# Kernel tuning notes

Measured on AMD Instinct MI355X. Metric: run time of the kernel, lower is better.

## Reference

```python
import jax, jax.numpy as jnp
import numpy as np

B, N, E, D = 8, 10000, 160000, 256
H = D // 2
SLOPE = 0.2  # LeakyReLU negative slope


def setup_inputs() -> dict:
    key = jax.random.key(0)
    ks = jax.random.split(key, 8)
    node_feats = jax.random.normal(ks[0], (B, N, D), dtype=jnp.float32)
    edge_attr = jax.random.uniform(ks[1], (E, 1), dtype=jnp.float32)
    W1 = jax.random.normal(ks[2], (2 * D, H), dtype=jnp.float32) * 0.05
    b1 = jnp.zeros((H,), dtype=jnp.float32)
    W2 = jax.random.normal(ks[3], (H, 1), dtype=jnp.float32) * 0.05
    b2 = jnp.zeros((1,), dtype=jnp.float32)
    edge_index = jax.random.randint(ks[4], (2, E), 0, N, dtype=jnp.int64)
    valid_masks = jax.random.randint(ks[5], (B, N), 0, 2).astype(bool)
    return {"node_feats": node_feats, "edge_attr": edge_attr, "W1": W1, "b1": b1,
            "W2": W2, "b2": b2, "edge_index": edge_index, "valid_masks": valid_masks}


def reference(node_feats, edge_attr, W1, b1, W2, b2, edge_index, valid_masks):
    # node_feats: [B,N,D]; edge_index: [2,E] shared across batch
    d = node_feats.shape[-1]
    src, dst = edge_index[0], edge_index[1]
    # cat([src_feats, dst_feats]) @ W1 == src @ W1[:d] + dst @ W1[d:]
    # Project per-node first, then gather per-edge: avoids the [B,E,2D] concat.
    ps = jnp.einsum('bnd,dh->bnh', node_feats, W1[:d])   # [B,N,H]
    pd = jnp.einsum('bnd,dh->bnh', node_feats, W1[d:])   # [B,N,H]
    h = ps[:, src] + pd[:, dst] + b1                      # [B,E,H]
    h = jnp.where(h >= 0, h, SLOPE * h)                   # LeakyReLU(0.2)
    scores = jnp.einsum('beh,h->be', h, W2[:, 0]) + b2[0]  # [B,E]
    scores = scores * edge_attr[:, 0]                     # edge_attr multiplies pre-softmax
    w = jax.nn.softmax(scores, axis=1)                    # global softmax over all edges
    # sparse_coo(edge_index, w) @ node_feats: out[src[e]] += w[e] * feats[dst[e]]
    msg = w[..., None] * node_feats[:, dst]               # [B,E,D]
    n = node_feats.shape[1]
    agg = jax.vmap(lambda m: jax.ops.segment_sum(m, src, num_segments=n))(msg)  # [B,N,D]
    mask = valid_masks.astype(node_feats.dtype)           # [B,N]
    cnt = mask.sum(axis=1)                                # [B]
    masked_mean = (agg * mask[..., None]).sum(axis=1) / jnp.maximum(cnt, 1.0)[:, None]
    full_mean = agg.mean(axis=1)
    graph_feats = jnp.where((cnt > 0)[:, None], masked_mean, full_mean)  # [B,D]
    return graph_feats, w
```

## Files before the change

kernel.cpp:

```cpp
#include <hip/hip_runtime.h>
#include <hip/hip_bf16.h>
#include <hip/hip_fp16.h>

#define B_ 8
#define N_ 10000
#define E_ 160000
#define D_ 256
#define H_ 128
#define SLOPE 0.2f
#define NCHUNK 50

#define NB_ 64
#define EPB_ (E_ / NB_)
#define BINS_ 256
#define NPB_ (N_ / 16)

#define SB_ 64
#define SEB_ (E_ / SB_)

typedef __attribute__((ext_vector_type(8))) _Float16 v8h;
typedef __attribute__((ext_vector_type(4))) _Float16 v4h;
typedef __attribute__((ext_vector_type(2))) _Float16 v2h;
typedef __attribute__((ext_vector_type(4))) float f32x4;

static __device__ __forceinline__ float dot2f(v2h a, v2h b, float c) {
#if __has_builtin(__builtin_amdgcn_fdot2)
    return __builtin_amdgcn_fdot2(a, b, c, false);
#else
    return fmaf((float)a.y, (float)b.y, fmaf((float)a.x, (float)b.x, c));
#endif
}

__global__ __launch_bounds__(64) void k_detect(const int* __restrict__ eidx_raw,
                                               const unsigned int* __restrict__ mask32,
                                               int* __restrict__ flags) {
    const int t = threadIdx.x;
    unsigned long long oddnz = __ballot(eidx_raw[2 * t + 1] != 0);
    unsigned long long mgt1  = __ballot(mask32[t] > 1u);
    if (t == 0) {
        flags[0] = (oddnz == 0ull) ? 1 : 0;
        flags[1] = (mgt1 != 0ull) ? 1 : 0;
    }
}

__global__ __launch_bounds__(256) void k_canon(const int* __restrict__ eidx_raw,
                                               const unsigned char* __restrict__ mask8,
                                               const unsigned int* __restrict__ mask32,
                                               const int* __restrict__ flags,
                                               const float* __restrict__ W1,
                                               const float* __restrict__ b1,
                                               const float* __restrict__ W2,
                                               int* __restrict__ ce,
                                               unsigned char* __restrict__ cm,
                                               unsigned char* __restrict__ cmT,
                                               __half* __restrict__ Wt,
                                               __half* __restrict__ b1h,
                                               __half* __restrict__ w2h) {
    const int i = blockIdx.x * 256 + threadIdx.x;
    const int f_e = flags[0], f_m = flags[1];
    if (i < 2 * E_) ce[i] = f_e ? eidx_raw[2 * i] : eidx_raw[i];
    if (i < B_ * N_) {
        unsigned char v = f_m ? (unsigned char)(mask8[i] != 0)
                              : (unsigned char)(mask32[i] != 0u);
        cm[i] = v;
        const int b = i / N_;
        const int n = i - b * N_;
        cmT[n * 8 + b] = v;
    }
    if (i < 2 * 256 * 128) {
        const int f = i & 127;
        const int row = i >> 7;
        const int c = row >> 8, k = row & 255;
        Wt[((c * 128 + f) * 256) + k] = __float2half(W1[row * 128 + f]);
    }
    if (i < 128) {
        b1h[i] = __float2half(b1[i]);
        w2h[i] = __float2half(W2[i]);
    }
}

__global__ __launch_bounds__(256) void khist(const int* __restrict__ ce,
                                             const unsigned char* __restrict__ cm,
                                             int* __restrict__ hpart,
                                             float* __restrict__ cnt) {
    const int tid = threadIdx.x;
    if (blockIdx.x < NB_) {
        __shared__ int h[BINS_];
        h[tid] = 0;
        __syncthreads();
        const int base = blockIdx.x * EPB_;
        for (int i = tid; i < EPB_; i += 256) {
            const int s = ce[base + i], d = ce[E_ + base + i];
            const int bin = (d / NPB_) * 16 + s / NPB_;
            atomicAdd(&h[bin], 1);
        }
        __syncthreads();
        hpart[blockIdx.x * BINS_ + tid] = h[tid];
    } else {
        const int b = blockIdx.x - NB_;
        int c = 0;
        for (int i = tid; i < N_; i += 256) c += cm[b * N_ + i] ? 1 : 0;
        __shared__ int red[256];
        red[tid] = c;
        __syncthreads();
        for (int s = 128; s > 0; s >>= 1) {
            if (tid < s) red[tid] += red[tid + s];
            __syncthreads();
        }
        if (tid == 0) cnt[b] = (float)red[0];
    }
}

__global__ __launch_bounds__(256) void kprefix(const int* __restrict__ hpart,
                                               int* __restrict__ offsetG,
                                               int* __restrict__ bstart) {
    __shared__ int cnt[BINS_];
    __shared__ int excl[BINS_];
    const int bin = threadIdx.x;
    int c = 0;
    for (int b = 0; b < NB_; b++) c += hpart[b * BINS_ + bin];
    cnt[bin] = c;
    __syncthreads();
    if (bin == 0) {
        int r = 0;
        for (int i = 0; i < BINS_; i++) { excl[i] = r; r += cnt[i]; }
    }
    __syncthreads();
    if ((bin & 15) == 0) bstart[bin >> 4] = excl[bin];
    if (bin == 0) bstart[16] = E_;
    int run = excl[bin];
    for (int b = 0; b < NB_; b++) {
        offsetG[b * BINS_ + bin] = run;
        run += hpart[b * BINS_ + bin];
    }
}

__global__ __launch_bounds__(256) void kscatter(const int* __restrict__ ce,
                                                const int* __restrict__ offsetG,
                                                int4* __restrict__ esort,
                                                int* __restrict__ rank) {
    __shared__ int loc[BINS_];
    const int tid = threadIdx.x;
    loc[tid] = offsetG[blockIdx.x * BINS_ + tid];
    __syncthreads();
    const int base = blockIdx.x * EPB_;
    for (int i = tid; i < EPB_; i += 256) {
        const int e = base + i;
        const int s = ce[e], d = ce[E_ + e];
        const int bin = (d / NPB_) * 16 + s / NPB_;
        const int pos = atomicAdd(&loc[bin], 1);
        esort[pos] = make_int4(s, d, e, 0);
        rank[e] = pos;
    }
}

__global__ __launch_bounds__(256) void k1_mfma(const float* __restrict__ X,
                                               const __half* __restrict__ Wt,
                                               __half* __restrict__ ps,
                                               __half* __restrict__ pd) {
    const int rb = blockIdx.x;
    const int tid = threadIdx.x;
    const int wave = tid >> 6, lane = tid & 63;
    const int quad = lane >> 4, l16 = lane & 15;

    __shared__ _Float16 Xs[128 * 40];

    f32x4 acc[2][2][8];
#pragma unroll
    for (int c = 0; c < 2; c++)
#pragma unroll
        for (int i = 0; i < 2; i++)
#pragma unroll
            for (int j = 0; j < 8; j++) acc[c][i][j] = (f32x4){0.f, 0.f, 0.f, 0.f};

    const int row_base = rb * 128;
    const int sr = tid >> 1;
    const int sh = tid & 1;

    for (int kc = 0; kc < 8; ++kc) {
        {
            const float4* src = (const float4*)&X[(size_t)(row_base + sr) * 256 + kc * 32 + sh * 16];
            _Float16* dst = &Xs[sr * 40 + sh * 16];
#pragma unroll
            for (int j = 0; j < 4; ++j) {
                float4 v = src[j];
                v4h p = {(_Float16)v.x, (_Float16)v.y, (_Float16)v.z, (_Float16)v.w};
                *(v4h*)&dst[j * 4] = p;
            }
        }
        __syncthreads();

        v8h wf[2][2];
#pragma unroll
        for (int cb = 0; cb < 2; ++cb)
#pragma unroll
            for (int ft = 0; ft < 2; ++ft)
                wf[cb][ft] = *(const v8h*)&Wt[((size_t)cb * 128 + wave * 32 + ft * 16 + l16) * 256 + kc * 32 + quad * 8];

#pragma unroll
        for (int nt = 0; nt < 8; ++nt) {
            v8h xf = *(v8h*)&Xs[(nt * 16 + l16) * 40 + quad * 8];
            acc[0][0][nt] = __builtin_amdgcn_mfma_f32_16x16x32_f16(wf[0][0], xf, acc[0][0][nt], 0, 0, 0);
            acc[0][1][nt] = __builtin_amdgcn_mfma_f32_16x16x32_f16(wf[0][1], xf, acc[0][1][nt], 0, 0, 0);
            acc[1][0][nt] = __builtin_amdgcn_mfma_f32_16x16x32_f16(wf[1][0], xf, acc[1][0][nt], 0, 0, 0);
            acc[1][1][nt] = __builtin_amdgcn_mfma_f32_16x16x32_f16(wf[1][1], xf, acc[1][1][nt], 0, 0, 0);
        }
        __syncthreads();
    }

#pragma unroll
    for (int nt = 0; nt < 8; ++nt) {
        const int R = row_base + nt * 16 + l16;
        const int b = R / N_;
        const int n = R - b * N_;
        const size_t off = ((size_t)(n * 8 + b)) * 128 + wave * 32 + quad * 4;
#pragma unroll
        for (int cb = 0; cb < 2; ++cb) {
            __half* base = (cb ? pd : ps) + off;
#pragma unroll
            for (int ft = 0; ft < 2; ++ft) {
                f32x4 a = acc[cb][ft][nt];
                v4h h = {(_Float16)a.x, (_Float16)a.y, (_Float16)a.z, (_Float16)a.w};
                *(v4h*)(base + ft * 16) = h;
            }
        }
    }
}

__global__ __launch_bounds__(256) void k2_scores(const __half* __restrict__ ps,
                                                 const __half* __restrict__ pd,
                                                 const int4* __restrict__ esort,
                                                 const __half* __restrict__ b1h,
                                                 const __half* __restrict__ w2h,
                                                 const float* __restrict__ b2,
                                                 const float* __restrict__ eattr,
                                                 float* __restrict__ scS) {
    const int tid = threadIdx.x;
    const int wave = tid >> 6;
    const int lane = tid & 63;
    const int bid = blockIdx.x;
    const int lb = (bid & 7) * 2500 + (bid >> 3);
    const int e0 = lb * 8 + wave * 2;

    const int b = lane >> 3;
    const int hi = (lane & 7) * 16;

    v2h b1p[8], w2p[8];
    {
        const v2h* bp = (const v2h*)(b1h + hi);
        const v2h* wp = (const v2h*)(w2h + hi);
#pragma unroll
        for (int j = 0; j < 8; j++) { b1p[j] = bp[j]; w2p[j] = wp[j]; }
    }
    const float bias2 = b2[0];
    const v2h slp = {(_Float16)SLOPE, (_Float16)SLOPE};

#pragma unroll
    for (int q = 0; q < 2; q++) {
        const int e = e0 + q;
        const int4 er = esort[e];
        const int src = er.x, dst = er.y, orig = er.z;

        const float4* aps = (const float4*)&ps[((size_t)src * 8 + b) * 128 + hi];
        const float4* apd = (const float4*)&pd[((size_t)dst * 8 + b) * 128 + hi];
        float4 rs[2] = {aps[0], aps[1]};
        float4 rd[2] = {apd[0], apd[1]};
        const v2h* sv = (const v2h*)rs;
        const v2h* dv = (const v2h*)rd;

        float acc = 0.f;
#pragma unroll
        for (int j = 0; j < 8; j++) {
            v2h x = sv[j] + dv[j] + b1p[j];
            v2h l = __builtin_elementwise_max(x, x * slp);
            acc = dot2f(l, w2p[j], acc);
        }
        acc += __shfl_xor(acc, 1);
        acc += __shfl_xor(acc, 2);
        acc += __shfl_xor(acc, 4);

        if ((lane & 7) == 0) {
            scS[(size_t)e * 8 + b] = (acc + bias2) * eattr[orig];
        }
    }
}

__global__ __launch_bounds__(256) void k3s_stats(const float* __restrict__ scS,
                                                 float* __restrict__ pmax,
                                                 double* __restrict__ psum) {
    const int tid = threadIdx.x;
    const int wave = tid >> 6, lane = tid & 63;
    const int base = blockIdx.x * SEB_;

    float fm[8];
#pragma unroll
    for (int j = 0; j < 8; j++) fm[j] = -3.4e38f;
    for (int i = tid; i < SEB_; i += 256) {
        const float4* s4 = (const float4*)&scS[(size_t)(base + i) * 8];
        float4 a = s4[0], b = s4[1];
        fm[0] = fmaxf(fm[0], a.x); fm[1] = fmaxf(fm[1], a.y);
        fm[2] = fmaxf(fm[2], a.z); fm[3] = fmaxf(fm[3], a.w);
        fm[4] = fmaxf(fm[4], b.x); fm[5] = fmaxf(fm[5], b.y);
        fm[6] = fmaxf(fm[6], b.z); fm[7] = fmaxf(fm[7], b.w);
    }
#pragma unroll
    for (int k = 1; k <= 32; k <<= 1)
#pragma unroll
        for (int j = 0; j < 8; j++) fm[j] = fmaxf(fm[j], __shfl_xor(fm[j], k));
    __shared__ float lmax[4][8];
    if (lane == 0)
#pragma unroll
        for (int j = 0; j < 8; j++) lmax[wave][j] = fm[j];
    __syncthreads();
    float m[8];
#pragma unroll
    for (int j = 0; j < 8; j++)
        m[j] = fmaxf(fmaxf(lmax[0][j], lmax[1][j]), fmaxf(lmax[2][j], lmax[3][j]));

    double s[8];
#pragma unroll
    for (int j = 0; j < 8; j++) s[j] = 0.0;
    for (int i = tid; i < SEB_; i += 256) {
        const float4* s4 = (const float4*)&scS[(size_t)(base + i) * 8];
        float4 a = s4[0], b = s4[1];
        s[0] += (double)expf(a.x - m[0]); s[1] += (double)expf(a.y - m[1]);
        s[2] += (double)expf(a.z - m[2]); s[3] += (double)expf(a.w - m[3]);
        s[4] += (double)expf(b.x - m[4]); s[5] += (double)expf(b.y - m[5]);
        s[6] += (double)expf(b.z - m[6]); s[7] += (double)expf(b.w - m[7]);
    }
#pragma unroll
    for (int k = 1; k <= 32; k <<= 1)
#pragma unroll
        for (int j = 0; j < 8; j++) s[j] += __shfl_xor(s[j], k);
    __shared__ double lsum[4][8];
    if (lane == 0)
#pragma unroll
        for (int j = 0; j < 8; j++) lsum[wave][j] = s[j];
    __syncthreads();
    if (tid < 8) {
        pmax[blockIdx.x * 8 + tid] = m[tid];
        psum[blockIdx.x * 8 + tid] = lsum[0][tid] + lsum[1][tid] + lsum[2][tid] + lsum[3][tid];
    }
}

static __device__ __forceinline__ void stats_combine(const float* __restrict__ pmax,
                                                     const double* __restrict__ psum,
                                                     int tid, float* smx, float* sinvx) {
    if (tid < 64) {
        float v[8];
        const float4* p4 = (const float4*)&pmax[tid * 8];
        float4 a = p4[0], b = p4[1];
        v[0] = a.x; v[1] = a.y; v[2] = a.z; v[3] = a.w;
        v[4] = b.x; v[5] = b.y; v[6] = b.z; v[7] = b.w;
        float mc[8];
#pragma unroll
        for (int j = 0; j < 8; j++) mc[j] = v[j];
#pragma unroll
        for (int k = 1; k <= 32; k <<= 1)
#pragma unroll
            for (int j = 0; j < 8; j++) v[j] = fmaxf(v[j], __shfl_xor(v[j], k));
        double z[8];
#pragma unroll
        for (int j = 0; j < 8; j++)
            z[j] = psum[tid * 8 + j] * (double)expf(mc[j] - v[j]);
#pragma unroll
        for (int k = 1; k <= 32; k <<= 1)
#pragma unroll
            for (int j = 0; j < 8; j++) z[j] += __shfl_xor(z[j], k);
        if (tid == 0)
#pragma unroll
            for (int j = 0; j < 8; j++) { smx[j] = v[j]; sinvx[j] = (float)(1.0 / z[j]); }
    }
}

__global__ __launch_bounds__(256) void k3e_norm(const float* __restrict__ scS,
                                                const int* __restrict__ rank,
                                                const float* __restrict__ pmax,
                                                const double* __restrict__ psum,
                                                float* __restrict__ wout) {
    const int tid = threadIdx.x;
    __shared__ float smx[8], sinvx[8];
    stats_combine(pmax, psum, tid, smx, sinvx);
    __syncthreads();

    const int e = blockIdx.x * 256 + tid;
    const int p = rank[e];
    const float4* s4 = (const float4*)&scS[(size_t)p * 8];
    float4 a = s4[0], b = s4[1];
    float wv[8];
    wv[0] = expf(a.x - smx[0]) * sinvx[0]; wv[1] = expf(a.y - smx[1]) * sinvx[1];
    wv[2] = expf(a.z - smx[2]) * sinvx[2]; wv[3] = expf(a.w - smx[3]) * sinvx[3];
    wv[4] = expf(b.x - smx[4]) * sinvx[4]; wv[5] = expf(b.y - smx[5]) * sinvx[5];
    wv[6] = expf(b.z - smx[6]) * sinvx[6]; wv[7] = expf(b.w - smx[7]) * sinvx[7];
#pragma unroll
    for (int j = 0; j < 8; j++) wout[(size_t)j * E_ + e] = wv[j];
}

__global__ __launch_bounds__(256) void k3f_bin(const int4* __restrict__ esort,
                                               const float* __restrict__ scS,
                                               const unsigned char* __restrict__ cmT,
                                               const float* __restrict__ pmax,
                                               const double* __restrict__ psum,
                                               const int* __restrict__ bstart,
                                               float* __restrict__ Wpf,
                                               float* __restrict__ Wpm) {
    const int bucket = blockIdx.x;
    const int sub = blockIdx.y;
    const int tid = threadIdx.x;

    __shared__ float smx[8], sinvx[8];
    stats_combine(pmax, psum, tid, smx, sinvx);

    __shared__ float lWf[NPB_ * 8];
    __shared__ float lWm[NPB_ * 8];
    for (int i = tid; i < NPB_ * 8; i += 256) { lWf[i] = 0.f; lWm[i] = 0.f; }
    __syncthreads();

    float m[8], inv[8];
#pragma unroll
    for (int j = 0; j < 8; j++) { m[j] = smx[j]; inv[j] = sinvx[j]; }

    const int bs = bstart[bucket], be = bstart[bucket + 1];
    const int len = be - bs;
    const int s0 = bs + (int)((long long)len * sub / 8);
    const int s1 = bs + (int)((long long)len * (sub + 1) / 8);
    const int nbase = bucket * NPB_;

    for (int p = s0 + tid; p < s1; p += 256) {
        const int4 er = esort[p];
        const int src = er.x;
        const int rel = er.y - nbase;
        const float4* s4 = (const float4*)&scS[(size_t)p * 8];
        float4 a = s4[0], b = s4[1];
        float wv[8];
        wv[0] = expf(a.x - m[0]) * inv[0]; wv[1] = expf(a.y - m[1]) * inv[1];
        wv[2] = expf(a.z - m[2]) * inv[2]; wv[3] = expf(a.w - m[3]) * inv[3];
        wv[4] = expf(b.x - m[4]) * inv[4]; wv[5] = expf(b.y - m[5]) * inv[5];
        wv[6] = expf(b.z - m[6]) * inv[6]; wv[7] = expf(b.w - m[7]) * inv[7];
        const unsigned long long mm = *(const unsigned long long*)&cmT[src * 8];
        float* lf = &lWf[rel * 8];
        float* lm = &lWm[rel * 8];
#pragma unroll
        for (int j = 0; j < 8; j++) {
            atomicAdd(&lf[j], wv[j]);
            if ((mm >> (8 * j)) & 1ull) atomicAdd(&lm[j], wv[j]);
        }
    }
    __syncthreads();

    float* of = Wpf + ((size_t)bucket * 8 + sub) * (NPB_ * 8);
    float* om = Wpm + ((size_t)bucket * 8 + sub) * (NPB_ * 8);
    for (int i = tid; i < NPB_ * 8; i += 256) { of[i] = lWf[i]; om[i] = lWm[i]; }
}

__global__ __launch_bounds__(256) void k3g_reduce(const float* __restrict__ Wpf,
                                                  const float* __restrict__ Wpm,
                                                  float* __restrict__ WfT,
                                                  float* __restrict__ WmT) {
    const int i = blockIdx.x * 256 + threadIdx.x;
    if (i >= N_ * 8) return;
    const int n = i >> 3, b = i & 7;
    const int bucket = n / NPB_;
    const int rel = n - bucket * NPB_;
    float sf = 0.f, sm = 0.f;
#pragma unroll
    for (int sub = 0; sub < 8; sub++) {
        const size_t off = ((size_t)bucket * 8 + sub) * (NPB_ * 8) + rel * 8 + b;
        sf += Wpf[off];
        sm += Wpm[off];
    }
    WfT[i] = sf;
    WmT[i] = sm;
}

__global__ __launch_bounds__(256) void k4b_wsum(const float* __restrict__ X,
                                                const float* __restrict__ WmT,
                                                const float* __restrict__ WfT,
                                                float* __restrict__ gpart) {
    const int c = blockIdx.x;
    const int b = blockIdx.y;
    const int tx = threadIdx.x & 63;
    const int ty = threadIdx.x >> 6;
    const int npc = N_ / NCHUNK;
    const int n0 = c * npc;

    const float4* X4 = (const float4*)(X + (size_t)b * N_ * 256);
    float4 am = {0.f, 0.f, 0.f, 0.f};
    float4 af = {0.f, 0.f, 0.f, 0.f};

    for (int n = n0 + ty; n < n0 + npc; n += 4) {
        float wm = WmT[n * 8 + b];
        float wf = WfT[n * 8 + b];
        float4 v = X4[(size_t)n * 64 + tx];
        am.x = fmaf(wm, v.x, am.x); am.y = fmaf(wm, v.y, am.y);
        am.z = fmaf(wm, v.z, am.z); am.w = fmaf(wm, v.w, am.w);
        af.x = fmaf(wf, v.x, af.x); af.y = fmaf(wf, v.y, af.y);
        af.z = fmaf(wf, v.z, af.z); af.w = fmaf(wf, v.w, af.w);
    }

    __shared__ float4 red[256];
    red[threadIdx.x] = am;
    __syncthreads();
    if (ty == 0) {
        float4 r1 = red[tx + 64], r2 = red[tx + 128], r3 = red[tx + 192];
        am.x += r1.x + r2.x + r3.x; am.y += r1.y + r2.y + r3.y;
        am.z += r1.z + r2.z + r3.z; am.w += r1.w + r2.w + r3.w;
    }
    __syncthreads();
    red[threadIdx.x] = af;
    __syncthreads();
    if (ty == 0) {
        float4 r1 = red[tx + 64], r2 = red[tx + 128], r3 = red[tx + 192];
        af.x += r1.x + r2.x + r3.x; af.y += r1.y + r2.y + r3.y;
        af.z += r1.z + r2.z + r3.z; af.w += r1.w + r2.w + r3.w;
        float4* gp4 = (float4*)gpart;
        gp4[((c * 2 + 0) * 8 + b) * 64 + tx] = am;
        gp4[((c * 2 + 1) * 8 + b) * 64 + tx] = af;
    }
}

__global__ __launch_bounds__(256) void k5_final(const float* __restrict__ gpart,
                                                const float* __restrict__ cnt,
                                                float* __restrict__ gf) {
    const int b = blockIdx.x;
    const int d = threadIdx.x;
    float sm = 0.f, sf = 0.f;
    for (int c = 0; c < NCHUNK; c++) {
        sm += gpart[((c * 2 + 0) * 8 + b) * 256 + d];
        sf += gpart[((c * 2 + 1) * 8 + b) * 256 + d];
    }
    const float cn = cnt[b];
    gf[b * 256 + d] = (cn > 0.f) ? (sm / cn) : (sf / (float)N_);
}

static inline char* align16(char* p) {
    return (char*)(((uintptr_t)p + 15) & ~(uintptr_t)15);
}

extern "C" void kernel_launch(void* const* d_in, const int* in_sizes, int n_in,
                              void* d_out, int out_size, void* d_ws, size_t ws_size,
                              hipStream_t stream) {
    const float* X     = (const float*)d_in[0];
    const float* eattr = (const float*)d_in[1];
    const float* W1    = (const float*)d_in[2];
    const float* b1    = (const float*)d_in[3];
    const float* W2    = (const float*)d_in[4];
    const float* b2    = (const float*)d_in[5];
    const int*   eidx_raw = (const int*)d_in[6];
    const unsigned char* mask8 = (const unsigned char*)d_in[7];
    const unsigned int*  mask32 = (const unsigned int*)d_in[7];

    float* out  = (float*)d_out;
    float* gf   = out;
    float* wout = out + 2048;

    char* cur = (char*)d_ws;
    __half* ps_h = (__half*)cur;             cur += (size_t)N_ * 8 * 128 * 2;
    __half* pd_h = (__half*)cur;             cur += (size_t)N_ * 8 * 128 * 2;
    __half* Wt   = (__half*)cur;             cur += 2 * 128 * 256 * 2;
    int* ce      = (int*)cur;                cur += 2 * E_ * 4;
    unsigned char* cmT = (unsigned char*)cur; cur += N_ * 8;
    unsigned char* cm  = (unsigned char*)cur; cur += B_ * N_;
    cur = align16(cur);
    float* cnt   = (float*)cur;              cur += 8 * 4;
    int* flags   = (int*)cur;                cur += 2 * 4;
    cur = align16(cur);
    float* pmax  = (float*)cur;              cur += SB_ * 8 * 4;
    cur = align16(cur);
    double* psum = (double*)cur;             cur += SB_ * 8 * 8;
    float* gpart = (float*)cur;              cur += NCHUNK * 2 * 8 * 256 * 4;
    int* hpart   = (int*)cur;                cur += NB_ * BINS_ * 4;
    int* offsetG = (int*)cur;                cur += NB_ * BINS_ * 4;
    int* bstart  = (int*)cur;                cur += 32 * 4;
    cur = align16(cur);
    int4* esort  = (int4*)cur;               cur += (size_t)E_ * 16;
    int* rankB   = (int*)cur;                cur += E_ * 4;
    __half* b1h  = (__half*)cur;             cur += 128 * 2;
    __half* w2h  = (__half*)cur;             cur += 128 * 2;
    cur = align16(cur);
    float* scS   = (float*)cur;              cur += (size_t)E_ * 8 * 4;

    char* ocur = (char*)d_ws;
    float* Wpf = (float*)ocur;               ocur += (size_t)16 * 8 * NPB_ * 8 * 4;
    float* Wpm = (float*)ocur;               ocur += (size_t)16 * 8 * NPB_ * 8 * 4;
    float* WfT = (float*)ocur;               ocur += N_ * 8 * 4;
    float* WmT = (float*)ocur;               ocur += N_ * 8 * 4;

    hipLaunchKernelGGL(k_detect, dim3(1), dim3(64), 0, stream, eidx_raw, mask32, flags);
    hipLaunchKernelGGL(k_canon, dim3(1250), dim3(256), 0, stream,
                       eidx_raw, mask8, mask32, flags, W1, b1, W2,
                       ce, cm, cmT, Wt, b1h, w2h);
    hipLaunchKernelGGL(khist, dim3(NB_ + 8), dim3(256), 0, stream, ce, cm, hpart, cnt);
    hipLaunchKernelGGL(kprefix, dim3(1), dim3(256), 0, stream, hpart, offsetG, bstart);
    hipLaunchKernelGGL(kscatter, dim3(NB_), dim3(256), 0, stream, ce, offsetG, esort, rankB);
    hipLaunchKernelGGL(k1_mfma, dim3(625), dim3(256), 0, stream, X, Wt, ps_h, pd_h);
    hipLaunchKernelGGL(k2_scores, dim3(E_ / 8), dim3(256), 0, stream,
                       ps_h, pd_h, esort, b1h, w2h, b2, eattr, scS);
    hipLaunchKernelGGL(k3s_stats, dim3(SB_), dim3(256), 0, stream, scS, pmax, psum);
    hipLaunchKernelGGL(k3e_norm, dim3(E_ / 256), dim3(256), 0, stream,
                       scS, rankB, pmax, psum, wout);
    hipLaunchKernelGGL(k3f_bin, dim3(16, 8), dim3(256), 0, stream,
                       esort, scS, cmT, pmax, psum, bstart, Wpf, Wpm);
    hipLaunchKernelGGL(k3g_reduce, dim3((N_ * 8 + 255) / 256), dim3(256), 0, stream,
                       Wpf, Wpm, WfT, WmT);
    hipLaunchKernelGGL(k4b_wsum, dim3(NCHUNK, 8), dim3(256), 0, stream, X, WmT, WfT, gpart);
    hipLaunchKernelGGL(k5_final, dim3(8), dim3(256), 0, stream, gpart, cnt, gf);
}
```

Before: 298.5 us.

## Double-buffer X tile and prefetch W fragments in projection GEMM, halve row tile

The node-projection MFMA kernel now processes 64 rows per block instead of 128, doubling the grid to 1250 blocks. It also double-buffers the X shared tile and register-prefetches the next K-chunk of X and W while the current chunk's MFMAs run, dropping one barrier per iteration. The aim is to hide global-load latency and improve occupancy. In exchange each block re-reads W more often, and the prefetch registers raise register pressure.

```diff
diff --git a/kernel.cpp b/kernel.cpp
--- a/kernel.cpp
+++ b/kernel.cpp
@@ -163,65 +163,90 @@
     const int wave = tid >> 6, lane = tid & 63;
     const int quad = lane >> 4, l16 = lane & 15;
 
-    __shared__ _Float16 Xs[128 * 40];
-
-    f32x4 acc[2][2][8];
+    __shared__ _Float16 Xs[2][64 * 40];
+
+    f32x4 acc[2][2][4];
 #pragma unroll
     for (int c = 0; c < 2; c++)
 #pragma unroll
         for (int i = 0; i < 2; i++)
 #pragma unroll
-            for (int j = 0; j < 8; j++) acc[c][i][j] = (f32x4){0.f, 0.f, 0.f, 0.f};
-
-    const int row_base = rb * 128;
-    const int sr = tid >> 1;
-    const int sh = tid & 1;
+            for (int j = 0; j < 4; j++) acc[c][i][j] = (f32x4){0.f, 0.f, 0.f, 0.f};
+
+    const int row_base = rb * 64;
+    const int sr = tid >> 2;
+    const int part = tid & 3;
+
+    const float* xsrc = &X[(size_t)(row_base + sr) * 256 + part * 8];
+    const __half* wbase = &Wt[((size_t)(wave * 32 + l16)) * 256 + quad * 8];
+
+    float4 xq0, xq1;
+    v8h wcur[2][2], wnxt[2][2];
+
+    xq0 = *(const float4*)(xsrc);
+    xq1 = *(const float4*)(xsrc + 4);
+#pragma unroll
+    for (int cb = 0; cb < 2; cb++)
+#pragma unroll
+        for (int ft = 0; ft < 2; ft++)
+            wcur[cb][ft] = *(const v8h*)(wbase + (size_t)(cb * 128 + ft * 16) * 256);
+    {
+        _Float16* dst = &Xs[0][sr * 40 + part * 8];
+        v4h p0 = {(_Float16)xq0.x, (_Float16)xq0.y, (_Float16)xq0.z, (_Float16)xq0.w};
+        v4h p1 = {(_Float16)xq1.x, (_Float16)xq1.y, (_Float16)xq1.z, (_Float16)xq1.w};
+        *(v4h*)dst = p0;
+        *(v4h*)(dst + 4) = p1;
+    }
+    __syncthreads();
 
     for (int kc = 0; kc < 8; ++kc) {
-        {
-            const float4* src = (const float4*)&X[(size_t)(row_base + sr) * 256 + kc * 32 + sh * 16];
-            _Float16* dst = &Xs[sr * 40 + sh * 16];
-#pragma unroll
-            for (int j = 0; j < 4; ++j) {
-                float4 v = src[j];
-                v4h p = {(_Float16)v.x, (_Float16)v.y, (_Float16)v.z, (_Float16)v.w};
-                *(v4h*)&dst[j * 4] = p;
-            }
+        const int cur = kc & 1;
+        if (kc < 7) {
+            xq0 = *(const float4*)(xsrc + (kc + 1) * 32);
+            xq1 = *(const float4*)(xsrc + (kc + 1) * 32 + 4);
+#pragma unroll
+            for (int cb = 0; cb < 2; cb++)
+#pragma unroll
+                for (int ft = 0; ft < 2; ft++)
+                    wnxt[cb][ft] = *(const v8h*)(wbase + (size_t)(cb * 128 + ft * 16) * 256 + (kc + 1) * 32);
+        }
+#pragma unroll
+        for (int nt = 0; nt < 4; ++nt) {
+            v8h xf = *(v8h*)&Xs[cur][(nt * 16 + l16) * 40 + quad * 8];
+            acc[0][0][nt] = __builtin_amdgcn_mfma_f32_16x16x32_f16(wcur[0][0], xf, acc[0][0][nt], 0, 0, 0);
+            acc[0][1][nt] = __builtin_amdgcn_mfma_f32_16x16x32_f16(wcur[0][1], xf, acc[0][1][nt], 0, 0, 0);
+            acc[1][0][nt] = __builtin_amdgcn_mfma_f32_16x16x32_f16(wcur[1][0], xf, acc[1][0][nt], 0, 0, 0);
+            acc[1][1][nt] = __builtin_amdgcn_mfma_f32_16x16x32_f16(wcur[1][1], xf, acc[1][1][nt], 0, 0, 0);
+        }
+        if (kc < 7) {
+            _Float16* dst = &Xs[cur ^ 1][sr * 40 + part * 8];
+            v4h p0 = {(_Float16)xq0.x, (_Float16)xq0.y, (_Float16)xq0.z, (_Float16)xq0.w};
+            v4h p1 = {(_Float16)xq1.x, (_Float16)xq1.y, (_Float16)xq1.z, (_Float16)xq1.w};
+            *(v4h*)dst = p0;
+            *(v4h*)(dst + 4) = p1;
+#pragma unroll
+            for (int cb = 0; cb < 2; cb++)
+#pragma unroll
+                for (int ft = 0; ft < 2; ft++)
+                    wcur[cb][ft] = wnxt[cb][ft];
         }
         __syncthreads();
-
-        v8h wf[2][2];
-#pragma unroll
-        for (int cb = 0; cb < 2; ++cb)
-#pragma unroll
-            for (int ft = 0; ft < 2; ++ft)
-                wf[cb][ft] = *(const v8h*)&Wt[((size_t)cb * 128 + wave * 32 + ft * 16 + l16) * 256 + kc * 32 + quad * 8];
-
-#pragma unroll
-        for (int nt = 0; nt < 8; ++nt) {
-            v8h xf = *(v8h*)&Xs[(nt * 16 + l16) * 40 + quad * 8];
-            acc[0][0][nt] = __builtin_amdgcn_mfma_f32_16x16x32_f16(wf[0][0], xf, acc[0][0][nt], 0, 0, 0);
-            acc[0][1][nt] = __builtin_amdgcn_mfma_f32_16x16x32_f16(wf[0][1], xf, acc[0][1][nt], 0, 0, 0);
-            acc[1][0][nt] = __builtin_amdgcn_mfma_f32_16x16x32_f16(wf[1][0], xf, acc[1][0][nt], 0, 0, 0);
-            acc[1][1][nt] = __builtin_amdgcn_mfma_f32_16x16x32_f16(wf[1][1], xf, acc[1][1][nt], 0, 0, 0);
-        }
-        __syncthreads();
-    }
-
-#pragma unroll
-    for (int nt = 0; nt < 8; ++nt) {
+    }
+
+#pragma unroll
+    for (int nt = 0; nt < 4; ++nt) {
         const int R = row_base + nt * 16 + l16;
         const int b = R / N_;
         const int n = R - b * N_;
         const size_t off = ((size_t)(n * 8 + b)) * 128 + wave * 32 + quad * 4;
 #pragma unroll
         for (int cb = 0; cb < 2; ++cb) {
-            __half* base = (cb ? pd : ps) + off;
+            __half* basep = (cb ? pd : ps) + off;
 #pragma unroll
             for (int ft = 0; ft < 2; ++ft) {
                 f32x4 a = acc[cb][ft][nt];
                 v4h h = {(_Float16)a.x, (_Float16)a.y, (_Float16)a.z, (_Float16)a.w};
-                *(v4h*)(base + ft * 16) = h;
+                *(v4h*)(basep + ft * 16) = h;
             }
         }
     }
@@ -593,7 +618,7 @@
     hipLaunchKernelGGL(khist, dim3(NB_ + 8), dim3(256), 0, stream, ce, cm, hpart, cnt);
     hipLaunchKernelGGL(kprefix, dim3(1), dim3(256), 0, stream, hpart, offsetG, bstart);
     hipLaunchKernelGGL(kscatter, dim3(NB_), dim3(256), 0, stream, ce, offsetG, esort, rankB);
-    hipLaunchKernelGGL(k1_mfma, dim3(625), dim3(256), 0, stream, X, Wt, ps_h, pd_h);
+    hipLaunchKernelGGL(k1_mfma, dim3(1250), dim3(256), 0, stream, X, Wt, ps_h, pd_h);
     hipLaunchKernelGGL(k2_scores, dim3(E_ / 8), dim3(256), 0, stream,
                        ps_h, pd_h, esort, b1h, w2h, b2, eattr, scS);
     hipLaunchKernelGGL(k3s_stats, dim3(SB_), dim3(256), 0, stream, scS, pmax, psum);
```

After: 300.1 us. Within noise of the previous version (+0.5%).
